# Performance work log

Hardware: AMD Instinct MI355X
Metric: run time of the kernel (lower is better)

## Reference

```python
import jax, jax.numpy as jnp
import numpy as np
from math import sqrt

B, L, S, H, E = 4, 2048, 2048, 8, 64
T = 1.0  # softmax temperature


def setup_inputs() -> dict:
    key = jax.random.key(0)
    kq, kk, kv = jax.random.split(key, 3)
    q = jax.random.normal(kq, (B, L, H, E), dtype=jnp.float32)
    k = jax.random.normal(kk, (B, S, H, E), dtype=jnp.float32)
    v = jax.random.normal(kv, (B, S, H, E), dtype=jnp.float32)
    mask = jnp.zeros((B, L), dtype=jnp.bool_)  # unused by the module, kept for signature fidelity
    return {"q": q, "k": k, "v": v, "mask": mask}


def reference(q, k, v, mask):
    Bq, Lq, Hq, Eq = q.shape
    # [B,L,H,E] -> [B,H,E,L]; FFT over time axis
    xq = jnp.transpose(q, (0, 2, 3, 1))
    xk = jnp.transpose(k, (0, 2, 3, 1))
    xv = jnpp_t = jnp.transpose(v, (0, 2, 3, 1))
    xq_ft = jnp.fft.rfft(xq, axis=-1, norm='ortho')   # [B,H,E,Lf]
    xk_ft = jnp.fft.rfft(xk, axis=-1, norm='ortho')   # [B,H,E,Sf]
    xv_ft = jnp.fft.rfft(xv, axis=-1, norm='ortho')   # [B,H,E,Sf]
    # complex frequency-domain scores [B,H,Lf,Sf]
    scores = jnp.einsum('bhex,bhey->bhxy', xq_ft, jnp.conj(xk_ft)) / sqrt(Eq)
    # activation == 'softmax': softmax over |scores|/T, then real-weighted complex mix
    attn = jax.nn.softmax(jnp.abs(scores) / T, axis=-1)
    xqkv_ft = jnp.einsum('bhxy,bhey->bhex', attn.astype(xv_ft.dtype), xv_ft)  # [B,H,E,Lf]
    out = jnp.fft.irfft(xqkv_ft, n=Lq, axis=-1, norm='ortho')  # [B,H,E,L]
    return jnp.transpose(out, (0, 3, 1, 2))  # [B,L,H,E]
```

## Files before the change

### kernel.cpp

```cpp
#include <hip/hip_runtime.h>
#include <hip/hip_bf16.h>
#include <math.h>

#define LOGN  11
#define NN    2048
#define LOGM  10
#define MM    1024
#define NF    1025
#define NYP   1056
#define TWO_PI 6.283185307179586f
#define INV_SQRT_N 0.022097086912079608f
#define INV_SCALE  0.044194173824159216f

typedef __attribute__((ext_vector_type(8))) short bhalf8;
typedef __attribute__((ext_vector_type(4))) float f32x4;

#define MFMA16(a, b, c) __builtin_amdgcn_mfma_f32_16x16x32_bf16(a, b, c, 0, 0, 0)

__device__ __forceinline__ unsigned short f2bf(float f) {
    union { float f; unsigned u; } v; v.f = f;
    unsigned r = v.u + 0x7FFFu + ((v.u >> 16) & 1u);
    return (unsigned short)(r >> 16);
}
__device__ __forceinline__ float bf2f(unsigned short h) {
    union { unsigned u; float f; } v; v.u = ((unsigned)h) << 16;
    return v.f;
}

__device__ __forceinline__ void fft_stages_m(float2* buf, const float2* tw, int tid)
{
    for (int st = 1; st <= LOGM; st++) {
        int half = 1 << (st - 1);
        #pragma unroll
        for (int it = 0; it < 2; it++) {
            int j   = tid + 256 * it;
            int pos = j & (half - 1);
            int grp = j >> (st - 1);
            int i0  = (grp << st) + pos;
            int i1  = i0 + half;
            float2 w = tw[pos << (LOGM - st)];
            float2 a = buf[i0];
            float2 b = buf[i1];
            float2 bw = make_float2(b.x * w.x - b.y * w.y,
                                    b.x * w.y + b.y * w.x);
            buf[i0] = make_float2(a.x + bw.x, a.y + bw.y);
            buf[i1] = make_float2(a.x - bw.x, a.y - bw.y);
        }
        __syncthreads();
    }
}

__global__ __launch_bounds__(256) void tr_fwd(const float* __restrict__ q,
                                              const float* __restrict__ k,
                                              const float* __restrict__ v,
                                              unsigned short* __restrict__ ttr)
{
    __shared__ float Ts[64][65];
    int tt     = blockIdx.x;
    int h      = blockIdx.y;
    int z      = blockIdx.z;
    int tensor = z >> 2;
    int b      = z & 3;
    int tid    = threadIdx.x;
    int t0     = tt * 64;

    const float* in = (tensor == 0) ? q : (tensor == 1) ? k : v;

    {
        int tl = tid >> 2, ec = (tid & 3) * 16;
        const float* src = in + ((size_t)b * 2048 + t0 + tl) * 512 + h * 64 + ec;
        #pragma unroll
        for (int m = 0; m < 4; m++) {
            float4 v4 = *(const float4*)(src + m * 4);
            Ts[tl][ec + m * 4 + 0] = v4.x;
            Ts[tl][ec + m * 4 + 1] = v4.y;
            Ts[tl][ec + m * 4 + 2] = v4.z;
            Ts[tl][ec + m * 4 + 3] = v4.w;
        }
    }
    __syncthreads();
    {
        int el = tid >> 2, tc = (tid & 3) * 16;
        size_t row = ((size_t)(tensor * 32 + b * 8 + h)) * 64 + el;
        unsigned short* dst = ttr + row * 2048 + t0 + tc;
        #pragma unroll
        for (int j = 0; j < 16; j++) dst[j] = f2bf(Ts[tc + j][el]);
    }
}

__global__ __launch_bounds__(256) void fft_fwd(const unsigned short* __restrict__ ttr,
                                               unsigned short* __restrict__ Pq,
                                               unsigned short* __restrict__ Pk,
                                               unsigned short* __restrict__ Pv)
{
    __shared__ float2 buf[MM];
    __shared__ float2 tw[MM / 2];

    int g      = blockIdx.x;
    int p      = g % 96;
    int e      = g / 96;
    int tensor = p / 32;
    int bh     = p % 32;
    int tid    = threadIdx.x;

    unsigned short* plane = (tensor == 0) ? Pq : (tensor == 1) ? Pk : Pv;

    for (int i = tid; i < MM / 2; i += 256) {
        float ang = -TWO_PI * (float)i / (float)MM;
        float sv, cv;
        __sincosf(ang, &sv, &cv);
        tw[i] = make_float2(cv, sv);
    }

    const unsigned short* src = ttr + ((size_t)p * 64 + e) * 2048;
    #pragma unroll
    for (int i = 0; i < 4; i++) {
        int j = tid + 256 * i;
        unsigned pr = *(const unsigned*)(src + 2 * j);
        float x0 = bf2f((unsigned short)(pr & 0xFFFFu));
        float x1 = bf2f((unsigned short)(pr >> 16));
        buf[__brev((unsigned)j) >> (32 - LOGM)] = make_float2(x0, x1);
    }
    __syncthreads();

    fft_stages_m(buf, tw, tid);

    unsigned short* dre = plane + ((size_t)bh * 128 + e) * NYP;
    unsigned short* dim_ = dre + (size_t)64 * NYP;

    for (int kk = tid; kk < NF; kk += 256) {
        float2 A  = buf[kk & (MM - 1)];
        float2 Bc = buf[(MM - kk) & (MM - 1)];
        float Ex = 0.5f * (A.x + Bc.x), Ey = 0.5f * (A.y - Bc.y);
        float Dx = 0.5f * (A.x - Bc.x), Dy = 0.5f * (A.y + Bc.y);
        float Ox = Dy, Oy = -Dx;
        float th = -(TWO_PI / (float)NN) * (float)kk;
        float sn, cs;
        __sincosf(th, &sn, &cs);
        float Xr = Ex + cs * Ox - sn * Oy;
        float Xi = Ey + cs * Oy + sn * Ox;
        dre[kk]  = f2bf(Xr * INV_SQRT_N);
        dim_[kk] = f2bf(Xi * INV_SQRT_N);
    }
    for (int y = NF + tid; y < NYP; y += 256) { dre[y] = 0; dim_[y] = 0; }
}

__global__ __launch_bounds__(256) void qkpack(const unsigned short* __restrict__ Pq,
                                              const unsigned short* __restrict__ Pk,
                                              unsigned short* __restrict__ Qp,
                                              unsigned short* __restrict__ Kp)
{
    __shared__ unsigned short Ts[32][136];
    int y0  = blockIdx.x * 32;
    int bh  = blockIdx.y;
    int tsr = blockIdx.z;
    int tid = threadIdx.x;

    const unsigned short* srcp = (tsr == 0) ? Pq : Pk;
    unsigned short* dstp       = (tsr == 0) ? Qp : Kp;

    {
        int kk = tid >> 1, seg = tid & 1;
        const unsigned short* sp = srcp + ((size_t)bh * 128 + kk) * NYP + y0 + seg * 16;
        #pragma unroll
        for (int j = 0; j < 16; j++) Ts[seg * 16 + j][kk] = sp[j];
    }
    __syncthreads();
    {
        int y = tid >> 3, c = tid & 7;
        unsigned short* dst = dstp + ((size_t)bh * NYP + y0 + y) * 128 + c * 16;
        #pragma unroll
        for (int j = 0; j < 16; j++) dst[j] = Ts[y][c * 16 + j];
    }
}

struct FlashShared {
    union {
        struct {
            unsigned short Ks[32][136];
            unsigned short Vs[128][40];
        } kv;
        unsigned short OutT[128][72];
    } u;
    unsigned short Ps[4][16][40];
};

__global__ __launch_bounds__(256) void flash_mfma(
    const unsigned short* __restrict__ Qp,
    const unsigned short* __restrict__ Kp,
    const unsigned short* __restrict__ Vt,
    unsigned short* __restrict__ numb,
    float* __restrict__ lbuf)
{
    __shared__ FlashShared S;

    int g    = blockIdx.x;
    int bh   = g & 31;
    int idx  = g >> 5;
    int half = idx / 17;
    int x0   = (idx % 17) * 64;
    int tid  = threadIdx.x;
    int w    = tid >> 6;
    int lane = tid & 63;
    int qd   = lane >> 4;
    int col  = lane & 15;

    int xrow = x0 + w * 16 + col;
    int xq   = min(xrow, 1024);
    const unsigned short* qb = Qp + ((size_t)bh * NYP + xq) * 128 + qd * 8;
    bhalf8 Are[4], Aim[4];
    #pragma unroll
    for (int ks = 0; ks < 4; ks++) Are[ks] = *(const bhalf8*)(qb + ks * 32);
    Aim[0] = Are[2];
    Aim[1] = Are[3];
    #pragma unroll
    for (int ks = 0; ks < 2; ks++) {
        bhalf8 t = Are[ks];
        unsigned* u = (unsigned*)&t;
        #pragma unroll
        for (int j = 0; j < 4; j++) u[j] ^= 0x80008000u;
        Aim[ks + 2] = t;
    }

    f32x4 O[8];
    #pragma unroll
    for (int n = 0; n < 8; n++) O[n] = (f32x4){0.f, 0.f, 0.f, 0.f};
    float Lacc[4] = {0.f, 0.f, 0.f, 0.f};

    const unsigned short* kpb = Kp + (size_t)bh * NYP * 128;
    const unsigned short* vtb = Vt + (size_t)bh * 128 * NYP;

    int yy = tid >> 3, c = tid & 7;
    int ee = tid >> 1, h = tid & 1;

    int yt0 = half * 17, yt1 = min(33, yt0 + 17);

    uint4 kc0, kc1, vc0, vc1;
    {
        const uint4* s4 = (const uint4*)(kpb + ((size_t)(yt0 * 32 + yy)) * 128 + c * 16);
        kc0 = s4[0]; kc1 = s4[1];
        const uint4* s5 = (const uint4*)(vtb + (size_t)ee * NYP + yt0 * 32 + h * 16);
        vc0 = s5[0]; vc1 = s5[1];
    }

    for (int yt = yt0; yt < yt1; yt++) {
        __syncthreads();
        *(uint4*)&S.u.kv.Ks[yy][c * 16]     = kc0;
        *(uint4*)&S.u.kv.Ks[yy][c * 16 + 8] = kc1;
        *(uint4*)&S.u.kv.Vs[ee][h * 16]     = vc0;
        *(uint4*)&S.u.kv.Vs[ee][h * 16 + 8] = vc1;
        __syncthreads();

        uint4 kn0, kn1, vn0, vn1;
        if (yt + 1 < yt1) {
            int y0n = (yt + 1) * 32;
            const uint4* s4 = (const uint4*)(kpb + ((size_t)(y0n + yy)) * 128 + c * 16);
            kn0 = s4[0]; kn1 = s4[1];
            const uint4* s5 = (const uint4*)(vtb + (size_t)ee * NYP + y0n + h * 16);
            vn0 = s5[0]; vn1 = s5[1];
        }

        f32x4 sre[2], sim[2];
        #pragma unroll
        for (int sc = 0; sc < 2; sc++) {
            sre[sc] = (f32x4){0.f, 0.f, 0.f, 0.f};
            sim[sc] = (f32x4){0.f, 0.f, 0.f, 0.f};
        }
        #pragma unroll
        for (int sc = 0; sc < 2; sc++)
            #pragma unroll
            for (int ks = 0; ks < 4; ks++) {
                bhalf8 bfrag = *(const bhalf8*)&S.u.kv.Ks[col + 16 * sc][ks * 32 + qd * 8];
                sre[sc] = MFMA16(Are[ks], bfrag, sre[sc]);
                sim[sc] = MFMA16(Aim[ks], bfrag, sim[sc]);
            }

        #pragma unroll
        for (int r = 0; r < 4; r++) {
            float re0 = sre[0][r], im0 = sim[0][r];
            float re1 = sre[1][r], im1 = sim[1][r];
            float p0 = __expf(0.125f * sqrtf(re0 * re0 + im0 * im0));
            float p1 = __expf(0.125f * sqrtf(re1 * re1 + im1 * im1));
            Lacc[r] += p0 + p1;
            S.Ps[w][qd * 4 + r][col]      = f2bf(p0);
            S.Ps[w][qd * 4 + r][col + 16] = f2bf(p1);
        }

        bhalf8 pa = *(const bhalf8*)&S.Ps[w][col][qd * 8];
        #pragma unroll
        for (int n = 0; n < 8; n++) {
            bhalf8 bv = *(const bhalf8*)&S.u.kv.Vs[n * 16 + col][qd * 8];
            O[n] = MFMA16(pa, bv, O[n]);
        }

        kc0 = kn0; kc1 = kn1; vc0 = vn0; vc1 = vn1;
    }

    size_t hofs = (size_t)half * 32 * NYP;
    #pragma unroll
    for (int r = 0; r < 4; r++) {
        float ls = Lacc[r];
        ls += __shfl_xor(ls, 1);
        ls += __shfl_xor(ls, 2);
        ls += __shfl_xor(ls, 4);
        ls += __shfl_xor(ls, 8);
        if (half == 1) ls -= 31.0f;
        int x = x0 + w * 16 + qd * 4 + r;
        if (x <= 1024 && col == 0) lbuf[hofs + (size_t)bh * NYP + x] = ls;
    }

    __syncthreads();
    #pragma unroll
    for (int r = 0; r < 4; r++)
        #pragma unroll
        for (int n = 0; n < 8; n++)
            S.u.OutT[n * 16 + col][w * 16 + qd * 4 + r] = f2bf(O[n][r]);
    __syncthreads();
    {
        int kk2 = tid >> 1, seg = tid & 1;
        int xg  = x0 + seg * 32;
        if (xg < NYP) {
            unsigned short* dst =
                numb + (((size_t)half * 32 + bh) * 128 + kk2) * NYP + xg;
            const unsigned short* srcl = &S.u.OutT[kk2][seg * 32];
            #pragma unroll
            for (int m = 0; m < 4; m++)
                *(uint4*)(dst + m * 8) = *(const uint4*)(srcl + m * 8);
        }
    }
}

__global__ __launch_bounds__(256) void fft_inv(const unsigned short* __restrict__ numb,
                                               const float* __restrict__ lbuf,
                                               float* __restrict__ st)
{
    __shared__ float2 buf[MM];
    __shared__ float2 tw[MM / 2];

    int s   = blockIdx.x;
    int e   = s & 63;
    int bh  = s >> 6;
    int tid = threadIdx.x;

    for (int i = tid; i < MM / 2; i += 256) {
        float ang = TWO_PI * (float)i / (float)MM;
        float sv, cv;
        __sincosf(ang, &sv, &cv);
        tw[i] = make_float2(cv, sv);
    }

    const size_t HS = (size_t)32 * 128 * NYP;
    const unsigned short* nbr = numb + ((size_t)bh * 128 + e) * NYP;
    const unsigned short* nbi = numb + ((size_t)bh * 128 + 64 + e) * NYP;
    const float* l0 = lbuf + (size_t)bh * NYP;
    const float* l1 = l0 + (size_t)32 * NYP;

    #pragma unroll
    for (int i = 0; i < 4; i++) {
        int kk = tid + 256 * i;
        int x1 = kk, x2 = 1024 - kk;
        float iv1 = 1.f / (l0[x1] + l1[x1]);
        float iv2 = 1.f / (l0[x2] + l1[x2]);
        float Ax = (bf2f(nbr[x1]) + bf2f(nbr[HS + x1])) * iv1;
        float Ay = (bf2f(nbi[x1]) + bf2f(nbi[HS + x1])) * iv1;
        float Bx = (bf2f(nbr[x2]) + bf2f(nbr[HS + x2])) * iv2;
        float By = -((bf2f(nbi[x2]) + bf2f(nbi[HS + x2])) * iv2);
        float Ex = 0.5f * (Ax + Bx), Ey = 0.5f * (Ay + By);
        float Dx = 0.5f * (Ax - Bx), Dy = 0.5f * (Ay - By);
        float th = (TWO_PI / (float)NN) * (float)kk;
        float sn, cs;
        __sincosf(th, &sn, &cs);
        float Ox = Dx * cs - Dy * sn;
        float Oy = Dx * sn + Dy * cs;
        buf[__brev((unsigned)kk) >> (32 - LOGM)] = make_float2(Ex - Oy, Ey + Ox);
    }
    __syncthreads();

    fft_stages_m(buf, tw, tid);

    float* dst = st + ((size_t)bh * 64 + e) * 2048;
    #pragma unroll
    for (int i = 0; i < 4; i++) {
        int j = tid + 256 * i;
        float2 z = buf[j];
        *(float2*)&dst[2 * j] = make_float2(z.x * INV_SCALE, z.y * INV_SCALE);
    }
}

__global__ __launch_bounds__(256) void out_tr(const float* __restrict__ st,
                                              float* __restrict__ out)
{
    __shared__ float Ts[64][65];
    int tt  = blockIdx.x;
    int h   = blockIdx.y;
    int b   = blockIdx.z;
    int tid = threadIdx.x;
    int bh  = b * 8 + h;

    {
        int e = tid >> 2, tc = (tid & 3) * 16;
        const float* src = st + ((size_t)bh * 64 + e) * 2048 + tt * 64 + tc;
        #pragma unroll
        for (int m = 0; m < 4; m++) {
            float4 v4 = *(const float4*)(src + m * 4);
            Ts[e][tc + m * 4 + 0] = v4.x;
            Ts[e][tc + m * 4 + 1] = v4.y;
            Ts[e][tc + m * 4 + 2] = v4.z;
            Ts[e][tc + m * 4 + 3] = v4.w;
        }
    }
    __syncthreads();
    {
        int t = tid >> 2, ec = (tid & 3) * 16;
        float* dst = out + (size_t)b * 2048 * 512 + (size_t)(tt * 64 + t) * 512
                     + h * 64 + ec;
        #pragma unroll
        for (int m = 0; m < 4; m++) {
            float4 v4;
            v4.x = Ts[ec + m * 4 + 0][t];
            v4.y = Ts[ec + m * 4 + 1][t];
            v4.z = Ts[ec + m * 4 + 2][t];
            v4.w = Ts[ec + m * 4 + 3][t];
            *(float4*)(dst + m * 4) = v4;
        }
    }
}

extern "C" void kernel_launch(void* const* d_in, const int* in_sizes, int n_in,
                              void* d_out, int out_size, void* d_ws, size_t ws_size,
                              hipStream_t stream)
{
    const float* q = (const float*)d_in[0];
    const float* k = (const float*)d_in[1];
    const float* v = (const float*)d_in[2];
    float* out = (float*)d_out;

    char* ws = (char*)d_ws;
    const size_t PL = (size_t)32 * 128 * NYP * sizeof(unsigned short);
    unsigned short* Pq = (unsigned short*)(ws);
    unsigned short* Pk = (unsigned short*)(ws + PL);
    unsigned short* Pv = (unsigned short*)(ws + 2 * PL);
    unsigned short* ttr = (unsigned short*)(ws + 3 * PL);
    unsigned short* Qp = (unsigned short*)(ws + 3 * PL);
    unsigned short* Kp = (unsigned short*)(ws + 4 * PL);
    unsigned short* numb = (unsigned short*)(ws);
    float* st   = (float*)(ws + 3 * PL);
    float* lbuf = (float*)(ws + 5 * PL);

    hipLaunchKernelGGL(tr_fwd, dim3(32, 8, 12), dim3(256), 0, stream,
                       q, k, v, ttr);
    hipLaunchKernelGGL(fft_fwd, dim3(3 * 2048), dim3(256), 0, stream,
                       ttr, Pq, Pk, Pv);
    hipLaunchKernelGGL(qkpack, dim3(33, 32, 2), dim3(256), 0, stream,
                       Pq, Pk, Qp, Kp);
    hipLaunchKernelGGL(flash_mfma, dim3(1088), dim3(256), 0, stream,
                       Qp, Kp, Pv, numb, lbuf);
    hipLaunchKernelGGL(fft_inv, dim3(2048), dim3(256), 0, stream,
                       numb, lbuf, st);
    hipLaunchKernelGGL(out_tr, dim3(32, 8, 4), dim3(256), 0, stream,
                       st, out);
}
```

Before: 233.1 us.

## Double-buffer K/V with direct global-to-LDS loads, swizzle layouts, packed bf16 converts

The flash kernel now uses global_load_lds to fill double-buffered K and V tiles in LDS, with explicit waitcnt and barriers so the loads overlap compute. The K and V layouts are XOR-swizzled, in the producer kernels and in the reads, to avoid bank conflicts. The 1/8 score scale is folded into the Q FFT output. The fp32 to bf16 conversions use the hardware v_cvt_pk_bf16_f32 instruction and vector stores, and the global reads and writes in qkpack are vectorized. These changes touch many kernels at once, and the hand-placed vmcnt and barrier sequence risks ordering bugs.

Result: faster. 216.5 us (-7.1%).

```diff
diff --git a/kernel.cpp b/kernel.cpp
--- a/kernel.cpp
+++ b/kernel.cpp
@@ -16,6 +16,14 @@
 typedef __attribute__((ext_vector_type(4))) float f32x4;
 
 #define MFMA16(a, b, c) __builtin_amdgcn_mfma_f32_16x16x32_bf16(a, b, c, 0, 0, 0)
+
+#define GLD16(gp, lp)                                                              \
+    __builtin_amdgcn_global_load_lds(                                              \
+        (const __attribute__((address_space(1))) void*)(gp),                       \
+        (__attribute__((address_space(3))) void*)(lp), 16, 0, 0)
+
+#define CVTPK(dst, lo, hi) \
+    asm("v_cvt_pk_bf16_f32 %0, %1, %2" : "=v"(dst) : "v"(lo), "v"(hi))
 
 __device__ __forceinline__ unsigned short f2bf(float f) {
     union { float f; unsigned u; } v; v.f = f;
@@ -84,7 +92,15 @@
         size_t row = ((size_t)(tensor * 32 + b * 8 + h)) * 64 + el;
         unsigned short* dst = ttr + row * 2048 + t0 + tc;
         #pragma unroll
-        for (int j = 0; j < 16; j++) dst[j] = f2bf(Ts[tc + j][el]);
+        for (int m = 0; m < 4; m++) {
+            float a0 = Ts[tc + m * 4 + 0][el], a1 = Ts[tc + m * 4 + 1][el];
+            float a2 = Ts[tc + m * 4 + 2][el], a3 = Ts[tc + m * 4 + 3][el];
+            unsigned u0, u1;
+            CVTPK(u0, a0, a1);
+            CVTPK(u1, a2, a3);
+            uint2 o; o.x = u0; o.y = u1;
+            *(uint2*)(dst + m * 4) = o;
+        }
     }
 }
 
@@ -104,6 +120,8 @@
     int tid    = threadIdx.x;
 
     unsigned short* plane = (tensor == 0) ? Pq : (tensor == 1) ? Pk : Pv;
+    float scl = (tensor == 0) ? (INV_SQRT_N * 0.125f) : INV_SQRT_N;
+    int vk3 = (tensor == 2) ? (((e >> 2) & 3) << 3) : 0;
 
     for (int i = tid; i < MM / 2; i += 256) {
         float ang = -TWO_PI * (float)i / (float)MM;
@@ -128,21 +146,50 @@
     unsigned short* dre = plane + ((size_t)bh * 128 + e) * NYP;
     unsigned short* dim_ = dre + (size_t)64 * NYP;
 
-    for (int kk = tid; kk < NF; kk += 256) {
-        float2 A  = buf[kk & (MM - 1)];
-        float2 Bc = buf[(MM - kk) & (MM - 1)];
-        float Ex = 0.5f * (A.x + Bc.x), Ey = 0.5f * (A.y - Bc.y);
-        float Dx = 0.5f * (A.x - Bc.x), Dy = 0.5f * (A.y + Bc.y);
-        float Ox = Dy, Oy = -Dx;
-        float th = -(TWO_PI / (float)NN) * (float)kk;
-        float sn, cs;
-        __sincosf(th, &sn, &cs);
-        float Xr = Ex + cs * Ox - sn * Oy;
-        float Xi = Ey + cs * Oy + sn * Ox;
-        dre[kk]  = f2bf(Xr * INV_SQRT_N);
-        dim_[kk] = f2bf(Xi * INV_SQRT_N);
-    }
-    for (int y = NF + tid; y < NYP; y += 256) { dre[y] = 0; dim_[y] = 0; }
+#define RPOINT(Ai, Bi, KKi, XR, XI) do {                                   \
+        float Ex = 0.5f * (Ai.x + Bi.x), Ey = 0.5f * (Ai.y - Bi.y);        \
+        float Dx = 0.5f * (Ai.x - Bi.x), Dy = 0.5f * (Ai.y + Bi.y);        \
+        float Ox = Dy, Oy = -Dx;                                           \
+        float th = -(TWO_PI / (float)NN) * (float)(KKi);                   \
+        float sn, cs; __sincosf(th, &sn, &cs);                             \
+        XR = (Ex + cs * Ox - sn * Oy) * scl;                               \
+        XI = (Ey + cs * Oy + sn * Ox) * scl;                               \
+    } while (0)
+
+    #pragma unroll
+    for (int i = 0; i < 2; i++) {
+        int kk = 2 * tid + 512 * i;
+        float2 A0 = buf[kk];
+        float2 B0 = buf[(MM - kk) & (MM - 1)];
+        float2 A1 = buf[kk + 1];
+        float2 B1 = buf[MM - kk - 1];
+        float Xr0, Xi0, Xr1, Xi1;
+        RPOINT(A0, B0, kk, Xr0, Xi0);
+        RPOINT(A1, B1, kk + 1, Xr1, Xi1);
+        unsigned ur, ui;
+        CVTPK(ur, Xr0, Xr1);
+        CVTPK(ui, Xi0, Xi1);
+        int ks = kk ^ vk3;
+        *(unsigned*)(dre + ks)  = ur;
+        *(unsigned*)(dim_ + ks) = ui;
+    }
+    if (tid < 16) {
+        unsigned ur = 0, ui = 0;
+        if (tid == 0) {
+            float2 A = buf[0];
+            float sn, cs;
+            __sincosf(-(TWO_PI / (float)NN) * 1024.0f, &sn, &cs);
+            float Xr = (A.x + cs * A.y) * scl;
+            float Xi = (sn * A.y) * scl;
+            float zz = 0.f;
+            CVTPK(ur, Xr, zz);
+            CVTPK(ui, Xi, zz);
+        }
+        int ks = (1024 + 2 * tid) ^ vk3;
+        *(unsigned*)(dre + ks)  = ur;
+        *(unsigned*)(dim_ + ks) = ui;
+    }
+#undef RPOINT
 }
 
 __global__ __launch_bounds__(256) void qkpack(const unsigned short* __restrict__ Pq,
@@ -162,23 +209,37 @@
     {
         int kk = tid >> 1, seg = tid & 1;
         const unsigned short* sp = srcp + ((size_t)bh * 128 + kk) * NYP + y0 + seg * 16;
-        #pragma unroll
-        for (int j = 0; j < 16; j++) Ts[seg * 16 + j][kk] = sp[j];
+        uint4 va = *(const uint4*)sp;
+        uint4 vb = *(const uint4*)(sp + 8);
+        const unsigned short* pa = (const unsigned short*)&va;
+        const unsigned short* pb = (const unsigned short*)&vb;
+        #pragma unroll
+        for (int j = 0; j < 8; j++) Ts[seg * 16 + j][kk] = pa[j];
+        #pragma unroll
+        for (int j = 0; j < 8; j++) Ts[seg * 16 + 8 + j][kk] = pb[j];
     }
     __syncthreads();
     {
         int y = tid >> 3, c = tid & 7;
-        unsigned short* dst = dstp + ((size_t)bh * NYP + y0 + y) * 128 + c * 16;
-        #pragma unroll
-        for (int j = 0; j < 16; j++) dst[j] = Ts[y][c * 16 + j];
+        uint4 lo = *(const uint4*)&Ts[y][c * 16];
+        uint4 hi = *(const uint4*)&Ts[y][c * 16 + 8];
+        char* rowb = (char*)(dstp + ((size_t)bh * NYP + y0 + y) * 128);
+        if (tsr == 0) {
+            *(uint4*)(rowb + c * 32)      = lo;
+            *(uint4*)(rowb + c * 32 + 16) = hi;
+        } else {
+            int s = y & 7;
+            *(uint4*)(rowb + (((2 * c)     ^ s) << 4)) = lo;
+            *(uint4*)(rowb + (((2 * c + 1) ^ s) << 4)) = hi;
+        }
     }
 }
 
 struct FlashShared {
     union {
         struct {
-            unsigned short Ks[32][136];
-            unsigned short Vs[128][40];
+            unsigned short Ks[2][32][128];
+            unsigned short Vs[2][128][32];
         } kv;
         unsigned short OutT[128][72];
     } u;
@@ -227,38 +288,50 @@
     for (int n = 0; n < 8; n++) O[n] = (f32x4){0.f, 0.f, 0.f, 0.f};
     float Lacc[4] = {0.f, 0.f, 0.f, 0.f};
 
-    const unsigned short* kpb = Kp + (size_t)bh * NYP * 128;
-    const unsigned short* vtb = Vt + (size_t)bh * 128 * NYP;
-
-    int yy = tid >> 3, c = tid & 7;
-    int ee = tid >> 1, h = tid & 1;
-
     int yt0 = half * 17, yt1 = min(33, yt0 + 17);
 
-    uint4 kc0, kc1, vc0, vc1;
-    {
-        const uint4* s4 = (const uint4*)(kpb + ((size_t)(yt0 * 32 + yy)) * 128 + c * 16);
-        kc0 = s4[0]; kc1 = s4[1];
-        const uint4* s5 = (const uint4*)(vtb + (size_t)ee * NYP + yt0 * 32 + h * 16);
-        vc0 = s5[0]; vc1 = s5[1];
+    const char* ksrc = (const char*)Kp
+        + ((size_t)bh * NYP + (size_t)yt0 * 32 + w * 8) * 256 + lane * 16;
+    const char* vbase = (const char*)Vt + (size_t)bh * 128 * (NYP * 2);
+    const char* vsrc0 = vbase + ((size_t)(w * 32) + (lane >> 2)) * (NYP * 2)
+                        + (size_t)yt0 * 64 + (lane & 3) * 16;
+    const char* vsrc1 = vsrc0 + (size_t)16 * (NYP * 2);
+
+    int sw = col & 7;
+    int kco[4];
+    #pragma unroll
+    for (int ks = 0; ks < 4; ks++) kco[ks] = ((ks * 4 + qd) ^ sw) * 8;
+    int vq = (qd ^ ((col >> 2) & 3)) * 8;
+
+    {
+        int pb = yt0 & 1;
+        GLD16(ksrc,         &S.u.kv.Ks[pb][w * 8][0]);
+        GLD16(ksrc + 1024,  &S.u.kv.Ks[pb][w * 8 + 4][0]);
+        GLD16(vsrc0,        &S.u.kv.Vs[pb][w * 32][0]);
+        GLD16(vsrc1,        &S.u.kv.Vs[pb][w * 32 + 16][0]);
+        ksrc += 8192; vsrc0 += 64; vsrc1 += 64;
     }
 
     for (int yt = yt0; yt < yt1; yt++) {
-        __syncthreads();
-        *(uint4*)&S.u.kv.Ks[yy][c * 16]     = kc0;
-        *(uint4*)&S.u.kv.Ks[yy][c * 16 + 8] = kc1;
-        *(uint4*)&S.u.kv.Vs[ee][h * 16]     = vc0;
-        *(uint4*)&S.u.kv.Vs[ee][h * 16 + 8] = vc1;
-        __syncthreads();
-
-        uint4 kn0, kn1, vn0, vn1;
+        int cb = yt & 1, nb = cb ^ 1;
         if (yt + 1 < yt1) {
-            int y0n = (yt + 1) * 32;
-            const uint4* s4 = (const uint4*)(kpb + ((size_t)(y0n + yy)) * 128 + c * 16);
-            kn0 = s4[0]; kn1 = s4[1];
-            const uint4* s5 = (const uint4*)(vtb + (size_t)ee * NYP + y0n + h * 16);
-            vn0 = s5[0]; vn1 = s5[1];
-        }
+            GLD16(ksrc,         &S.u.kv.Ks[nb][w * 8][0]);
+            GLD16(ksrc + 1024,  &S.u.kv.Ks[nb][w * 8 + 4][0]);
+            GLD16(vsrc0,        &S.u.kv.Vs[nb][w * 32][0]);
+            GLD16(vsrc1,        &S.u.kv.Vs[nb][w * 32 + 16][0]);
+            ksrc += 8192; vsrc0 += 64; vsrc1 += 64;
+            __builtin_amdgcn_sched_barrier(0);
+            asm volatile("s_waitcnt vmcnt(4)" ::: "memory");
+        } else {
+            __builtin_amdgcn_sched_barrier(0);
+            asm volatile("s_waitcnt vmcnt(0)" ::: "memory");
+        }
+        __builtin_amdgcn_sched_barrier(0);
+        __builtin_amdgcn_s_barrier();
+        __builtin_amdgcn_sched_barrier(0);
+
+        const unsigned short* k0 = &S.u.kv.Ks[cb][col][0];
+        const unsigned short* k1 = &S.u.kv.Ks[cb][col + 16][0];
 
         f32x4 sre[2], sim[2];
         #pragma unroll
@@ -266,34 +339,44 @@
             sre[sc] = (f32x4){0.f, 0.f, 0.f, 0.f};
             sim[sc] = (f32x4){0.f, 0.f, 0.f, 0.f};
         }
-        #pragma unroll
-        for (int sc = 0; sc < 2; sc++)
-            #pragma unroll
-            for (int ks = 0; ks < 4; ks++) {
-                bhalf8 bfrag = *(const bhalf8*)&S.u.kv.Ks[col + 16 * sc][ks * 32 + qd * 8];
-                sre[sc] = MFMA16(Are[ks], bfrag, sre[sc]);
-                sim[sc] = MFMA16(Aim[ks], bfrag, sim[sc]);
-            }
+        __builtin_amdgcn_s_setprio(1);
+        #pragma unroll
+        for (int ks = 0; ks < 4; ks++) {
+            bhalf8 b0 = *(const bhalf8*)(k0 + kco[ks]);
+            bhalf8 b1 = *(const bhalf8*)(k1 + kco[ks]);
+            sre[0] = MFMA16(Are[ks], b0, sre[0]);
+            sim[0] = MFMA16(Aim[ks], b0, sim[0]);
+            sre[1] = MFMA16(Are[ks], b1, sre[1]);
+            sim[1] = MFMA16(Aim[ks], b1, sim[1]);
+        }
+        __builtin_amdgcn_s_setprio(0);
 
         #pragma unroll
         for (int r = 0; r < 4; r++) {
             float re0 = sre[0][r], im0 = sim[0][r];
             float re1 = sre[1][r], im1 = sim[1][r];
-            float p0 = __expf(0.125f * sqrtf(re0 * re0 + im0 * im0));
-            float p1 = __expf(0.125f * sqrtf(re1 * re1 + im1 * im1));
+            float p0 = __expf(__builtin_amdgcn_sqrtf(fmaf(re0, re0, im0 * im0)));
+            float p1 = __expf(__builtin_amdgcn_sqrtf(fmaf(re1, re1, im1 * im1)));
             Lacc[r] += p0 + p1;
-            S.Ps[w][qd * 4 + r][col]      = f2bf(p0);
-            S.Ps[w][qd * 4 + r][col + 16] = f2bf(p1);
+            unsigned up;
+            CVTPK(up, p0, p1);
+            S.Ps[w][qd * 4 + r][col]      = (unsigned short)up;
+            S.Ps[w][qd * 4 + r][col + 16] = (unsigned short)(up >> 16);
         }
 
         bhalf8 pa = *(const bhalf8*)&S.Ps[w][col][qd * 8];
+        __builtin_amdgcn_s_setprio(1);
         #pragma unroll
         for (int n = 0; n < 8; n++) {
-            bhalf8 bv = *(const bhalf8*)&S.u.kv.Vs[n * 16 + col][qd * 8];
+            bhalf8 bv = *(const bhalf8*)&S.u.kv.Vs[cb][n * 16 + col][vq];
             O[n] = MFMA16(pa, bv, O[n]);
         }
-
-        kc0 = kn0; kc1 = kn1; vc0 = vn0; vc1 = vn1;
+        __builtin_amdgcn_s_setprio(0);
+
+        asm volatile("s_waitcnt lgkmcnt(0)" ::: "memory");
+        __builtin_amdgcn_sched_barrier(0);
+        __builtin_amdgcn_s_barrier();
+        __builtin_amdgcn_sched_barrier(0);
     }
 
     size_t hofs = (size_t)half * 32 * NYP;
@@ -311,10 +394,13 @@
 
     __syncthreads();
     #pragma unroll
-    for (int r = 0; r < 4; r++)
-        #pragma unroll
-        for (int n = 0; n < 8; n++)
-            S.u.OutT[n * 16 + col][w * 16 + qd * 4 + r] = f2bf(O[n][r]);
+    for (int n = 0; n < 8; n++) {
+        unsigned u0, u1;
+        CVTPK(u0, O[n][0], O[n][1]);
+        CVTPK(u1, O[n][2], O[n][3]);
+        *(unsigned*)&S.u.OutT[n * 16 + col][w * 16 + qd * 4]     = u0;
+        *(unsigned*)&S.u.OutT[n * 16 + col][w * 16 + qd * 4 + 2] = u1;
+    }
     __syncthreads();
     {
         int kk2 = tid >> 1, seg = tid & 1;
```
